# Kernel tuning notes

Measured on AMD Instinct MI355X. Metric: run time of the kernel, lower is better.

The kernel has to match this reference:

```python
import jax, jax.numpy as jnp
import numpy as np

H = 16          # hidden_size
L = 24          # num_layers
LEN_TRAIN = 96
LEN_PRED = 48
B = 256         # leading dim of input (acts as TIME axis for the LSTMs, see notes)


def setup_inputs() -> dict:
    key = jax.random.key(0)
    ks = jax.random.split(key, 16)
    s = 1.0 / np.sqrt(H)  # PyTorch LSTM/Linear init scale
    u = lambda k, shp: jax.random.uniform(k, shp, jnp.float32, -s, s)
    return {
        "x": jax.random.normal(ks[0], (B, 1, LEN_TRAIN), jnp.float32),
        # lstm1: layer0 input_size=1, layers 1..23 input_size=2H
        "W_ih0_1": u(ks[1], (2, 4 * H, 1)),
        "W_ih_1": u(ks[2], (L - 1, 2, 4 * H, 2 * H)),
        "W_hh_1": u(ks[3], (L, 2, 4 * H, H)),
        "b_ih_1": u(ks[4], (L, 2, 4 * H)),
        "b_hh_1": u(ks[5], (L, 2, 4 * H)),
        # lstm2: all layers input_size=2H
        "W_ih_2": u(ks[6], (L, 2, 4 * H, 2 * H)),
        "W_hh_2": u(ks[7], (L, 2, 4 * H, H)),
        "b_ih_2": u(ks[8], (L, 2, 4 * H)),
        "b_hh_2": u(ks[9], (L, 2, 4 * H)),
        "fc1_w": u(ks[10], (1000, 2 * LEN_PRED * H)),
        "fc1_b": u(ks[11], (1000,)),
        "fc2_w": u(ks[12], (LEN_PRED, 1000)),
        "fc2_b": u(ks[13], (LEN_PRED,)),
    }


def _lstm_dir(x, Wih, Whh, bih, bhh, reverse):
    # x: (T, N, in). Precompute input-gate GEMM over whole sequence.
    xg = jnp.einsum("tni,gi->tng", x, Wih) + bih + bhh  # (T, N, 4H)

    def step(carry, g_in):
        h, c = carry
        g = g_in + h @ Whh.T
        i, f, gg, o = jnp.split(g, 4, axis=-1)  # PyTorch gate order i,f,g,o
        c = jax.nn.sigmoid(f) * c + jax.nn.sigmoid(i) * jnp.tanh(gg)
        h = jax.nn.sigmoid(o) * jnp.tanh(c)
        return (h, c), h

    N = x.shape[1]
    init = (jnp.zeros((N, H), x.dtype), jnp.zeros((N, H), x.dtype))
    _, hs = jax.lax.scan(step, init, xg, reverse=reverse)
    return hs  # (T, N, H), in original time order


def _bilstm_stack(x, Wih_per_layer, Whh, bih, bhh):
    for l in range(Whh.shape[0]):
        Wih = Wih_per_layer[l]
        fwd = _lstm_dir(x, Wih[0], Whh[l, 0], bih[l, 0], bhh[l, 0], False)
        bwd = _lstm_dir(x, Wih[1], Whh[l, 1], bih[l, 1], bhh[l, 1], True)
        x = jnp.concatenate([fwd, bwd], axis=-1)  # (T, N, 2H)
    return x


def reference(x, W_ih0_1, W_ih_1, W_hh_1, b_ih_1, b_hh_1,
              W_ih_2, W_hh_2, b_ih_2, b_hh_2,
              fc1_w, fc1_b, fc2_w, fc2_b):
    xp = jnp.transpose(x, (0, 2, 1))  # (B, 96, 1); dim0 is the LSTM time axis (batch_first=False quirk)
    wih1 = [W_ih0_1] + [W_ih_1[i] for i in range(L - 1)]
    h = _bilstm_stack(xp, wih1, W_hh_1, b_ih_1, b_hh_1)      # (B, 96, 2H)
    x1 = h[:, -LEN_PRED:, :]                                  # (B, 48, 2H)
    wih2 = [W_ih_2[i] for i in range(L)]
    h2 = _bilstm_stack(x1, wih2, W_hh_2, b_ih_2, b_hh_2)      # (B, 48, 2H)
    z = h2 + x1
    flat = z.reshape(z.shape[0], -1)                          # (B, 1536)
    y = jax.nn.relu(flat @ fc1_w.T + fc1_b) @ fc2_w.T + fc2_b # (B, 48)
    return jnp.transpose(y.reshape(y.shape[0], LEN_PRED, 1), (0, 2, 1))  # (B, 1, 48)
```

## Files before the change

### kernel.cpp

```cpp
#include <hip/hip_runtime.h>


template <int SEL>
__device__ __forceinline__ float quad_bcast(float v) {
  return __int_as_float(__builtin_amdgcn_update_dpp(
      0, __float_as_int(v), SEL * 0x55, 0xF, 0xF, true));
}

template <int IN_SZ, int N>
__global__ __launch_bounds__(256) void lstm_layer(
    const float* __restrict__ xin, float* __restrict__ xout,
    const float* __restrict__ Wih, const float* __restrict__ Whh,
    const float* __restrict__ bih, const float* __restrict__ bhh,
    int t_stride, int n_off) {
  __shared__ float xg[256 * 64];

  const int tid = threadIdx.x;
  const int lane = tid & 63;
  const int w = tid >> 6;
  const int d = blockIdx.x / N;
  const int n = blockIdx.x % N;

  {
    const int r = lane;
    const float bias = bih[d * 64 + r] + bhh[d * 64 + r];
    if constexpr (IN_SZ == 1) {
      const float xv =
          xin[(size_t)(w * 64 + lane) * t_stride + (n + n_off)];
      const float wih0 = Wih[d * 64 + r];
      const int xvb = __float_as_int(xv);
      for (int ti = 0; ti < 64; ++ti) {
        const float xs = __int_as_float(__builtin_amdgcn_readlane(xvb, ti));
        xg[(w * 64 + ti) * 64 + r] = fmaf(wih0, xs, bias);
      }
    } else {
      const int r8 = lane >> 3;
      const int c = lane & 7;
      const float* gbase = xin + (size_t)(n + n_off) * 32 + c * 4;
      float4 v[8];
#pragma unroll
      for (int i = 0; i < 8; ++i) {
        const int t = w * 64 + i * 8 + r8;
        v[i] = *reinterpret_cast<const float4*>(gbase + (size_t)t * t_stride);
      }
#pragma unroll
      for (int i = 0; i < 8; ++i) {
        const int t = w * 64 + i * 8 + r8;
        *reinterpret_cast<float4*>(&xg[t * 64 + 32 + c * 4]) = v[i];
      }
      float wih[32];
      const float4* wp =
          reinterpret_cast<const float4*>(Wih + (size_t)(d * 64 + r) * 32);
#pragma unroll
      for (int q = 0; q < 8; ++q) {
        const float4 t4 = wp[q];
        wih[4 * q + 0] = t4.x;
        wih[4 * q + 1] = t4.y;
        wih[4 * q + 2] = t4.z;
        wih[4 * q + 3] = t4.w;
      }
      for (int ti = 0; ti < 64; ++ti) {
        const int t = w * 64 + ti;
        const float4* xr = reinterpret_cast<const float4*>(&xg[t * 64 + 32]);
        float a0 = bias, a1 = 0.f, a2 = 0.f, a3 = 0.f;
#pragma unroll
        for (int q = 0; q < 8; ++q) {
          const float4 xv = xr[q];
          a0 = fmaf(wih[4 * q + 0], xv.x, a0);
          a1 = fmaf(wih[4 * q + 1], xv.y, a1);
          a2 = fmaf(wih[4 * q + 2], xv.z, a2);
          a3 = fmaf(wih[4 * q + 3], xv.w, a3);
        }
        xg[t * 64 + r] = (a0 + a1) + (a2 + a3);
      }
    }
  }
  __syncthreads();

  if (w == 0) {
    const int j = lane >> 2;
    const int g = lane & 3;
    const int r = g * 16 + j;

    float whh[16];
#pragma unroll
    for (int k = 0; k < 16; ++k) whh[k] = Whh[(d * 64 + r) * 16 + k];

    const float s_ = (g == 2) ? 2.885390082f : -1.442695041f;
    const float m_ = (g == 2) ? -2.0f : 1.0f;
    const float b_ = (g == 2) ? 1.0f : 0.0f;

    float hs[16];
#pragma unroll
    for (int k = 0; k < 16; ++k) hs[k] = 0.f;
    float c = 0.f;

    const int dt = d ? -1 : 1;
    int t = d ? 255 : 0;
    float cur0 = xg[t * 64 + r];
    float cur1 = xg[(t + dt) * 64 + r];

#define LSTM_STEP(CUR, TT)                                              \
  {                                                                     \
    float a0 = (CUR), a1 = 0.f, a2 = 0.f, a3 = 0.f;                     \
    _Pragma("unroll") for (int k = 0; k < 16; k += 4) {                 \
      a0 = fmaf(whh[k + 0], hs[k + 0], a0);                             \
      a1 = fmaf(whh[k + 1], hs[k + 1], a1);                             \
      a2 = fmaf(whh[k + 2], hs[k + 2], a2);                             \
      a3 = fmaf(whh[k + 3], hs[k + 3], a3);                             \
    }                                                                   \
    const float gv = (a0 + a1) + (a2 + a3);                             \
    const float e = __builtin_amdgcn_exp2f(s_ * gv);                    \
    const float v = fmaf(m_, __builtin_amdgcn_rcpf(1.0f + e), b_);      \
    const float si = quad_bcast<0>(v);                                  \
    const float sf = quad_bcast<1>(v);                                  \
    const float tg = quad_bcast<2>(v);                                  \
    const float so = quad_bcast<3>(v);                                  \
    c = fmaf(sf, c, si * tg);                                           \
    const float e2 = __builtin_amdgcn_exp2f(2.885390082f * c);          \
    const float th = fmaf(-2.0f, __builtin_amdgcn_rcpf(1.0f + e2), 1.0f); \
    const float h = so * th;                                            \
    xg[(TT)*64 + lane] = h;    \
    const int hb = __float_as_int(h);                                   \
    _Pragma("unroll") for (int k = 0; k < 16; ++k) hs[k] =              \
        __int_as_float(__builtin_amdgcn_readlane(hb, 4 * k));           \
  }

    for (int tt = 0; tt < 256; tt += 2) {
      const float nx0 = xg[((t + 2 * dt) & 255) * 64 + r];
      LSTM_STEP(cur0, t)
      const float nx1 = xg[((t + 3 * dt) & 255) * 64 + r];
      LSTM_STEP(cur1, t + dt)
      cur0 = nx0;
      cur1 = nx1;
      t += 2 * dt;
    }
#undef LSTM_STEP
  }
  __syncthreads();

  {
    const int q4 = tid & 3;
    const int tb = tid >> 2;
#pragma unroll
    for (int p = 0; p < 4; ++p) {
      const int t = p * 64 + tb;
      float4 v;
      v.x = xg[t * 64 + 16 * q4 + 0];
      v.y = xg[t * 64 + 16 * q4 + 4];
      v.z = xg[t * 64 + 16 * q4 + 8];
      v.w = xg[t * 64 + 16 * q4 + 12];
      *reinterpret_cast<float4*>(xout + ((size_t)t * N + n) * 32 + d * 16 +
                                 q4 * 4) = v;
    }
  }
}

__global__ __launch_bounds__(256) void fc1_kernel(
    const float* __restrict__ h2,
    const float* __restrict__ x1b,
    const float* __restrict__ w1, const float* __restrict__ b1,
    float* __restrict__ y1) {
  __shared__ float Zs[16][68];
  __shared__ float Ws[16][68];
  const int tid = threadIdx.x;
  const int m0 = blockIdx.x * 64;
  const int b0 = blockIdx.y * 64;
  const int rr = tid >> 2;
  const int c4 = (tid & 3) * 4;
  const int tx = tid & 15, ty = tid >> 4;

  float acc[4][4];
#pragma unroll
  for (int i = 0; i < 4; ++i)
#pragma unroll
    for (int jj = 0; jj < 4; ++jj) acc[i][jj] = 0.f;

  const bool wvalid = (m0 + rr) < 1000;
  const float* zr = h2 + (size_t)(b0 + rr) * 1536 + c4;
  const float* zr2 = x1b + (size_t)(b0 + rr) * 3072 + 1536 + c4;
  const float* wr = w1 + (size_t)(m0 + rr) * 1536 + c4;

  float4 za = *reinterpret_cast<const float4*>(zr);
  float4 zb = *reinterpret_cast<const float4*>(zr2);
  float4 wv = wvalid ? *reinterpret_cast<const float4*>(wr)
                     : make_float4(0.f, 0.f, 0.f, 0.f);

  for (int k0 = 0; k0 < 1536; k0 += 16) {
    Zs[c4 + 0][rr] = za.x + zb.x;
    Zs[c4 + 1][rr] = za.y + zb.y;
    Zs[c4 + 2][rr] = za.z + zb.z;
    Zs[c4 + 3][rr] = za.w + zb.w;
    Ws[c4 + 0][rr] = wv.x;
    Ws[c4 + 1][rr] = wv.y;
    Ws[c4 + 2][rr] = wv.z;
    Ws[c4 + 3][rr] = wv.w;
    if (k0 + 16 < 1536) {
      za = *reinterpret_cast<const float4*>(zr + k0 + 16);
      zb = *reinterpret_cast<const float4*>(zr2 + k0 + 16);
      if (wvalid) wv = *reinterpret_cast<const float4*>(wr + k0 + 16);
    }
    __syncthreads();
#pragma unroll
    for (int kk = 0; kk < 16; ++kk) {
      const float4 av = *reinterpret_cast<const float4*>(&Zs[kk][ty * 4]);
      const float4 bv = *reinterpret_cast<const float4*>(&Ws[kk][tx * 4]);
      const float a_[4] = {av.x, av.y, av.z, av.w};
      const float b_[4] = {bv.x, bv.y, bv.z, bv.w};
#pragma unroll
      for (int i = 0; i < 4; ++i)
#pragma unroll
        for (int jj = 0; jj < 4; ++jj)
          acc[i][jj] = fmaf(a_[i], b_[jj], acc[i][jj]);
    }
    __syncthreads();
  }
#pragma unroll
  for (int i = 0; i < 4; ++i) {
    const int b = b0 + ty * 4 + i;
#pragma unroll
    for (int jj = 0; jj < 4; ++jj) {
      const int m = m0 + tx * 4 + jj;
      if (m < 1000) {
        float vo = acc[i][jj] + b1[m];
        y1[(size_t)b * 1000 + m] = vo > 0.f ? vo : 0.f;
      }
    }
  }
}

__global__ __launch_bounds__(64) void fc2_kernel(
    const float* __restrict__ y1, const float* __restrict__ w2,
    const float* __restrict__ b2, float* __restrict__ out) {
  __shared__ float ys[1000];
  const int b = blockIdx.x;
  for (int k = threadIdx.x; k < 1000; k += 64) ys[k] = y1[(size_t)b * 1000 + k];
  __syncthreads();
  const int p = threadIdx.x;
  if (p < 48) {
    float a0 = b2[p], a1 = 0.f, a2 = 0.f, a3 = 0.f;
    const float* wr = w2 + (size_t)p * 1000;
    for (int k = 0; k < 1000; k += 4) {
      const float4 wv = *reinterpret_cast<const float4*>(wr + k);
      a0 = fmaf(ys[k + 0], wv.x, a0);
      a1 = fmaf(ys[k + 1], wv.y, a1);
      a2 = fmaf(ys[k + 2], wv.z, a2);
      a3 = fmaf(ys[k + 3], wv.w, a3);
    }
    out[(size_t)b * 48 + p] = (a0 + a1) + (a2 + a3);
  }
}

extern "C" void kernel_launch(void* const* d_in, const int* in_sizes, int n_in,
                              void* d_out, int out_size, void* d_ws,
                              size_t ws_size, hipStream_t stream) {
  const float* x = (const float*)d_in[0];
  const float* W_ih0_1 = (const float*)d_in[1];
  const float* W_ih_1 = (const float*)d_in[2];
  const float* W_hh_1 = (const float*)d_in[3];
  const float* b_ih_1 = (const float*)d_in[4];
  const float* b_hh_1 = (const float*)d_in[5];
  const float* W_ih_2 = (const float*)d_in[6];
  const float* W_hh_2 = (const float*)d_in[7];
  const float* b_ih_2 = (const float*)d_in[8];
  const float* b_hh_2 = (const float*)d_in[9];
  const float* fc1_w = (const float*)d_in[10];
  const float* fc1_b = (const float*)d_in[11];
  const float* fc2_w = (const float*)d_in[12];
  const float* fc2_b = (const float*)d_in[13];

  float* ws = (float*)d_ws;
  float* buf0 = ws;
  float* buf1 = ws + 786432;
  float* y1 = ws + 2 * 786432;
  float* q0 = buf0;
  float* q1 = buf0 + 393216;

  lstm_layer<1, 96><<<192, 256, 0, stream>>>(x, buf0, W_ih0_1, W_hh_1, b_ih_1,
                                             b_hh_1, 96, 0);
  for (int l = 1; l < 24; ++l) {
    const float* in = (l & 1) ? buf0 : buf1;
    float* outb = (l & 1) ? buf1 : buf0;
    lstm_layer<32, 96><<<192, 256, 0, stream>>>(
        in, outb, W_ih_1 + (size_t)(l - 1) * 4096, W_hh_1 + (size_t)l * 2048,
        b_ih_1 + l * 128, b_hh_1 + l * 128, 3072, 0);
  }
  lstm_layer<32, 48><<<96, 256, 0, stream>>>(buf1, q0, W_ih_2, W_hh_2, b_ih_2,
                                             b_hh_2, 3072, 48);
  for (int l = 1; l < 24; ++l) {
    const float* in = (l & 1) ? q0 : q1;
    float* outb = (l & 1) ? q1 : q0;
    lstm_layer<32, 48><<<96, 256, 0, stream>>>(
        in, outb, W_ih_2 + (size_t)l * 4096, W_hh_2 + (size_t)l * 2048,
        b_ih_2 + l * 128, b_hh_2 + l * 128, 1536, 0);
  }
  fc1_kernel<<<dim3(16, 4), 256, 0, stream>>>(q1, buf1, fc1_w, fc1_b, y1);
  fc2_kernel<<<256, 64, 0, stream>>>(y1, fc2_w, fc2_b, (float*)d_out);
}
```

Before: 2.238 ms.

## Fuse all LSTM layers into one persistent kernel and compute only needed columns

Replaces 48 per-layer LSTM launches with a single kernel where each block handles one of the 48 columns actually consumed downstream, running both directions and all layers with activations kept in LDS. Input-gate projections for the next layer are computed in-block from LDS instead of reloading from global memory. This removes launch overhead, global round trips, and the unused half of the first stack's columns, at the cost of only 48 blocks of parallelism.

Measured after the change: 3.063 ms. 1.37x slower.

```diff
diff --git a/kernel.cpp b/kernel.cpp
--- a/kernel.cpp
+++ b/kernel.cpp
@@ -7,158 +7,204 @@
       0, __float_as_int(v), SEL * 0x55, 0xF, 0xF, true));
 }
 
-template <int IN_SZ, int N>
-__global__ __launch_bounds__(256) void lstm_layer(
-    const float* __restrict__ xin, float* __restrict__ xout,
-    const float* __restrict__ Wih, const float* __restrict__ Whh,
-    const float* __restrict__ bih, const float* __restrict__ bhh,
-    int t_stride, int n_off) {
-  __shared__ float xg[256 * 64];
+__global__ __launch_bounds__(512) void lstm_fused(
+    const float* __restrict__ x, const float* __restrict__ W_ih0_1,
+    const float* __restrict__ W_ih_1, const float* __restrict__ W_hh_1,
+    const float* __restrict__ b_ih_1, const float* __restrict__ b_hh_1,
+    const float* __restrict__ W_ih_2, const float* __restrict__ W_hh_2,
+    const float* __restrict__ b_ih_2, const float* __restrict__ b_hh_2,
+    float* __restrict__ x1out, float* __restrict__ h2out) {
+  __shared__ float xgF[256 * 64];
+  __shared__ float xgB[256 * 64];
 
   const int tid = threadIdx.x;
   const int lane = tid & 63;
   const int w = tid >> 6;
-  const int d = blockIdx.x / N;
-  const int n = blockIdx.x % N;
+  const int np = blockIdx.x;
+  const int nglob = 48 + np;
 
   {
+    const int d = w >> 2;
+    const int wv = w & 3;
+    float* xg = d ? xgB : xgF;
     const int r = lane;
-    const float bias = bih[d * 64 + r] + bhh[d * 64 + r];
-    if constexpr (IN_SZ == 1) {
-      const float xv =
-          xin[(size_t)(w * 64 + lane) * t_stride + (n + n_off)];
-      const float wih0 = Wih[d * 64 + r];
-      const int xvb = __float_as_int(xv);
-      for (int ti = 0; ti < 64; ++ti) {
-        const float xs = __int_as_float(__builtin_amdgcn_readlane(xvb, ti));
-        xg[(w * 64 + ti) * 64 + r] = fmaf(wih0, xs, bias);
-      }
-    } else {
-      const int r8 = lane >> 3;
-      const int c = lane & 7;
-      const float* gbase = xin + (size_t)(n + n_off) * 32 + c * 4;
-      float4 v[8];
-#pragma unroll
-      for (int i = 0; i < 8; ++i) {
-        const int t = w * 64 + i * 8 + r8;
-        v[i] = *reinterpret_cast<const float4*>(gbase + (size_t)t * t_stride);
-      }
-#pragma unroll
-      for (int i = 0; i < 8; ++i) {
-        const int t = w * 64 + i * 8 + r8;
-        *reinterpret_cast<float4*>(&xg[t * 64 + 32 + c * 4]) = v[i];
-      }
-      float wih[32];
-      const float4* wp =
-          reinterpret_cast<const float4*>(Wih + (size_t)(d * 64 + r) * 32);
-#pragma unroll
-      for (int q = 0; q < 8; ++q) {
-        const float4 t4 = wp[q];
-        wih[4 * q + 0] = t4.x;
-        wih[4 * q + 1] = t4.y;
-        wih[4 * q + 2] = t4.z;
-        wih[4 * q + 3] = t4.w;
-      }
-      for (int ti = 0; ti < 64; ++ti) {
-        const int t = w * 64 + ti;
-        const float4* xr = reinterpret_cast<const float4*>(&xg[t * 64 + 32]);
-        float a0 = bias, a1 = 0.f, a2 = 0.f, a3 = 0.f;
+    const float bias = b_ih_1[d * 64 + r] + b_hh_1[d * 64 + r];
+    const float wih0 = W_ih0_1[d * 64 + r];
+    const int xvb =
+        __float_as_int(x[(size_t)(wv * 64 + lane) * 96 + nglob]);
+    for (int ti = 0; ti < 64; ++ti) {
+      const float xs = __int_as_float(__builtin_amdgcn_readlane(xvb, ti));
+      xg[(wv * 64 + ti) * 64 + r] = fmaf(wih0, xs, bias);
+    }
+  }
+  __syncthreads();
+
+  for (int L = 0; L < 48; ++L) {
+    if ((w & 3) == 0) {
+      const int d = w >> 2;
+      float* xg = d ? xgB : xgF;
+      const int j = lane >> 2;
+      const int g = lane & 3;
+      const int r = g * 16 + j;
+
+      const float* WhhP =
+          ((L < 24) ? (W_hh_1 + (size_t)L * 2048)
+                    : (W_hh_2 + (size_t)(L - 24) * 2048)) +
+          (size_t)d * 1024 + (size_t)r * 16;
+      float whh[16];
+#pragma unroll
+      for (int k = 0; k < 16; ++k) whh[k] = WhhP[k];
+
+      const float s_ = (g == 2) ? 2.885390082f : -1.442695041f;
+      const float m_ = (g == 2) ? -2.0f : 1.0f;
+      const float b_ = (g == 2) ? 1.0f : 0.0f;
+
+      float hs[16];
+#pragma unroll
+      for (int k = 0; k < 16; ++k) hs[k] = 0.f;
+      float c = 0.f;
+
+      const int dt = d ? -1 : 1;
+      int t = d ? 255 : 0;
+      float cur0 = xg[t * 64 + r];
+      float cur1 = xg[(t + dt) * 64 + r];
+
+#define LSTM_STEP(CUR, TT)                                                \
+  {                                                                       \
+    float a0 = (CUR), a1 = 0.f, a2 = 0.f, a3 = 0.f;                       \
+    _Pragma("unroll") for (int k = 0; k < 16; k += 4) {                   \
+      a0 = fmaf(whh[k + 0], hs[k + 0], a0);                               \
+      a1 = fmaf(whh[k + 1], hs[k + 1], a1);                               \
+      a2 = fmaf(whh[k + 2], hs[k + 2], a2);                               \
+      a3 = fmaf(whh[k + 3], hs[k + 3], a3);                               \
+    }                                                                     \
+    const float gv = (a0 + a1) + (a2 + a3);                               \
+    const float e = __builtin_amdgcn_exp2f(s_ * gv);                      \
+    const float v = fmaf(m_, __builtin_amdgcn_rcpf(1.0f + e), b_);        \
+    const float si = quad_bcast<0>(v);                                    \
+    const float sf = quad_bcast<1>(v);                                    \
+    const float tg = quad_bcast<2>(v);                                    \
+    const float so = quad_bcast<3>(v);                                    \
+    c = fmaf(sf, c, si * tg);                                             \
+    const float e2 = __builtin_amdgcn_exp2f(2.885390082f * c);            \
+    const float th = fmaf(-2.0f, __builtin_amdgcn_rcpf(1.0f + e2), 1.0f); \
+    const float h = so * th;                                              \
+    xg[(TT)*64 + r] = h;  \
+    const int hb = __float_as_int(h);                                     \
+    _Pragma("unroll") for (int k = 0; k < 16; ++k) hs[k] =                \
+        __int_as_float(__builtin_amdgcn_readlane(hb, 4 * k));             \
+  }
+
+      for (int tt = 0; tt < 256; tt += 2) {
+        const float nx0 = xg[((t + 2 * dt) & 255) * 64 + r];
+        LSTM_STEP(cur0, t)
+        const float nx1 = xg[((t + 3 * dt) & 255) * 64 + r];
+        LSTM_STEP(cur1, t + dt)
+        cur0 = nx0;
+        cur1 = nx1;
+        t += 2 * dt;
+      }
+#undef LSTM_STEP
+    }
+    __syncthreads();
+
+    if (L == 23 || L == 47) {
+      float* dst = (L == 23) ? x1out : h2out;
+#pragma unroll
+      for (int p = 0; p < 4; ++p) {
+        const int gi = p * 512 + tid;
+        const int t = gi >> 3;
+        const int cc = gi & 7;
+        const float* src = (cc < 4) ? &xgF[t * 64 + cc * 4]
+                                    : &xgB[t * 64 + (cc - 4) * 4];
+        const float4 v = *reinterpret_cast<const float4*>(src);
+        *reinterpret_cast<float4*>(dst + ((size_t)t * 48 + np) * 32 +
+                                   cc * 4) = v;
+      }
+      if (L == 47) break;
+      __syncthreads();
+    }
+
+    {
+      const int M = L + 1;
+      const float* WihP;
+      const float* bihP;
+      const float* bhhP;
+      if (M < 24) {
+        WihP = W_ih_1 + (size_t)(M - 1) * 4096;
+        bihP = b_ih_1 + (size_t)M * 128;
+        bhhP = b_hh_1 + (size_t)M * 128;
+      } else {
+        WihP = W_ih_2 + (size_t)(M - 24) * 4096;
+        bihP = b_ih_2 + (size_t)(M - 24) * 128;
+        bhhP = b_hh_2 + (size_t)(M - 24) * 128;
+      }
+      const int r = lane;
+      const float biasF = bihP[r] + bhhP[r];
+      const float biasB = bihP[64 + r] + bhhP[64 + r];
+
+      float wf[32], wb[32];
+      {
+        const float4* pf =
+            reinterpret_cast<const float4*>(WihP + (size_t)r * 32);
+        const float4* pb =
+            reinterpret_cast<const float4*>(WihP + 2048 + (size_t)r * 32);
 #pragma unroll
         for (int q = 0; q < 8; ++q) {
-          const float4 xv = xr[q];
-          a0 = fmaf(wih[4 * q + 0], xv.x, a0);
-          a1 = fmaf(wih[4 * q + 1], xv.y, a1);
-          a2 = fmaf(wih[4 * q + 2], xv.z, a2);
-          a3 = fmaf(wih[4 * q + 3], xv.w, a3);
+          const float4 a = pf[q];
+          wf[4 * q + 0] = a.x;
+          wf[4 * q + 1] = a.y;
+          wf[4 * q + 2] = a.z;
+          wf[4 * q + 3] = a.w;
+          const float4 b = pb[q];
+          wb[4 * q + 0] = b.x;
+          wb[4 * q + 1] = b.y;
+          wb[4 * q + 2] = b.z;
+          wb[4 * q + 3] = b.w;
         }
-        xg[t * 64 + r] = (a0 + a1) + (a2 + a3);
-      }
-    }
-  }
-  __syncthreads();
-
-  if (w == 0) {
-    const int j = lane >> 2;
-    const int g = lane & 3;
-    const int r = g * 16 + j;
-
-    float whh[16];
-#pragma unroll
-    for (int k = 0; k < 16; ++k) whh[k] = Whh[(d * 64 + r) * 16 + k];
-
-    const float s_ = (g == 2) ? 2.885390082f : -1.442695041f;
-    const float m_ = (g == 2) ? -2.0f : 1.0f;
-    const float b_ = (g == 2) ? 1.0f : 0.0f;
-
-    float hs[16];
-#pragma unroll
-    for (int k = 0; k < 16; ++k) hs[k] = 0.f;
-    float c = 0.f;
-
-    const int dt = d ? -1 : 1;
-    int t = d ? 255 : 0;
-    float cur0 = xg[t * 64 + r];
-    float cur1 = xg[(t + dt) * 64 + r];
-
-#define LSTM_STEP(CUR, TT)                                              \
-  {                                                                     \
-    float a0 = (CUR), a1 = 0.f, a2 = 0.f, a3 = 0.f;                     \
-    _Pragma("unroll") for (int k = 0; k < 16; k += 4) {                 \
-      a0 = fmaf(whh[k + 0], hs[k + 0], a0);                             \
-      a1 = fmaf(whh[k + 1], hs[k + 1], a1);                             \
-      a2 = fmaf(whh[k + 2], hs[k + 2], a2);                             \
-      a3 = fmaf(whh[k + 3], hs[k + 3], a3);                             \
-    }                                                                   \
-    const float gv = (a0 + a1) + (a2 + a3);                             \
-    const float e = __builtin_amdgcn_exp2f(s_ * gv);                    \
-    const float v = fmaf(m_, __builtin_amdgcn_rcpf(1.0f + e), b_);      \
-    const float si = quad_bcast<0>(v);                                  \
-    const float sf = quad_bcast<1>(v);                                  \
-    const float tg = quad_bcast<2>(v);                                  \
-    const float so = quad_bcast<3>(v);                                  \
-    c = fmaf(sf, c, si * tg);                                           \
-    const float e2 = __builtin_amdgcn_exp2f(2.885390082f * c);          \
-    const float th = fmaf(-2.0f, __builtin_amdgcn_rcpf(1.0f + e2), 1.0f); \
-    const float h = so * th;                                            \
-    xg[(TT)*64 + lane] = h;    \
-    const int hb = __float_as_int(h);                                   \
-    _Pragma("unroll") for (int k = 0; k < 16; ++k) hs[k] =              \
-        __int_as_float(__builtin_amdgcn_readlane(hb, 4 * k));           \
-  }
-
-    for (int tt = 0; tt < 256; tt += 2) {
-      const float nx0 = xg[((t + 2 * dt) & 255) * 64 + r];
-      LSTM_STEP(cur0, t)
-      const float nx1 = xg[((t + 3 * dt) & 255) * 64 + r];
-      LSTM_STEP(cur1, t + dt)
-      cur0 = nx0;
-      cur1 = nx1;
-      t += 2 * dt;
-    }
-#undef LSTM_STEP
-  }
-  __syncthreads();
-
-  {
-    const int q4 = tid & 3;
-    const int tb = tid >> 2;
-#pragma unroll
-    for (int p = 0; p < 4; ++p) {
-      const int t = p * 64 + tb;
-      float4 v;
-      v.x = xg[t * 64 + 16 * q4 + 0];
-      v.y = xg[t * 64 + 16 * q4 + 4];
-      v.z = xg[t * 64 + 16 * q4 + 8];
-      v.w = xg[t * 64 + 16 * q4 + 12];
-      *reinterpret_cast<float4*>(xout + ((size_t)t * N + n) * 32 + d * 16 +
-                                 q4 * 4) = v;
-    }
+      }
+
+      for (int ti = 0; ti < 32; ++ti) {
+        const int t = w * 32 + ti;
+        const float4* qf = reinterpret_cast<const float4*>(&xgF[t * 64]);
+        const float4* qb = reinterpret_cast<const float4*>(&xgB[t * 64]);
+        float xv[32];
+#pragma unroll
+        for (int q = 0; q < 4; ++q) {
+          const float4 a = qf[q];
+          xv[4 * q + 0] = a.x;
+          xv[4 * q + 1] = a.y;
+          xv[4 * q + 2] = a.z;
+          xv[4 * q + 3] = a.w;
+          const float4 b = qb[q];
+          xv[16 + 4 * q + 0] = b.x;
+          xv[16 + 4 * q + 1] = b.y;
+          xv[16 + 4 * q + 2] = b.z;
+          xv[16 + 4 * q + 3] = b.w;
+        }
+        float f0 = biasF, f1 = 0.f, f2 = 0.f, f3 = 0.f;
+        float g0 = biasB, g1 = 0.f, g2 = 0.f, g3 = 0.f;
+#pragma unroll
+        for (int k = 0; k < 32; k += 4) {
+          f0 = fmaf(wf[k + 0], xv[k + 0], f0);
+          f1 = fmaf(wf[k + 1], xv[k + 1], f1);
+          f2 = fmaf(wf[k + 2], xv[k + 2], f2);
+          f3 = fmaf(wf[k + 3], xv[k + 3], f3);
+          g0 = fmaf(wb[k + 0], xv[k + 0], g0);
+          g1 = fmaf(wb[k + 1], xv[k + 1], g1);
+          g2 = fmaf(wb[k + 2], xv[k + 2], g2);
+          g3 = fmaf(wb[k + 3], xv[k + 3], g3);
+        }
+        xgF[t * 64 + lane] = (f0 + f1) + (f2 + f3);
+        xgB[t * 64 + lane] = (g0 + g1) + (g2 + g3);
+      }
+    }
+    __syncthreads();
   }
 }
 
 __global__ __launch_bounds__(256) void fc1_kernel(
-    const float* __restrict__ h2,
-    const float* __restrict__ x1b,
+    const float* __restrict__ h2, const float* __restrict__ x1b,
     const float* __restrict__ w1, const float* __restrict__ b1,
     float* __restrict__ y1) {
   __shared__ float Zs[16][68];
@@ -178,7 +224,7 @@
 
   const bool wvalid = (m0 + rr) < 1000;
   const float* zr = h2 + (size_t)(b0 + rr) * 1536 + c4;
-  const float* zr2 = x1b + (size_t)(b0 + rr) * 3072 + 1536 + c4;
+  const float* zr2 = x1b + (size_t)(b0 + rr) * 1536 + c4;
   const float* wr = w1 + (size_t)(m0 + rr) * 1536 + c4;
 
   float4 za = *reinterpret_cast<const float4*>(zr);
@@ -270,30 +316,13 @@
   const float* fc2_b = (const float*)d_in[13];
 
   float* ws = (float*)d_ws;
-  float* buf0 = ws;
-  float* buf1 = ws + 786432;
-  float* y1 = ws + 2 * 786432;
-  float* q0 = buf0;
-  float* q1 = buf0 + 393216;
-
-  lstm_layer<1, 96><<<192, 256, 0, stream>>>(x, buf0, W_ih0_1, W_hh_1, b_ih_1,
-                                             b_hh_1, 96, 0);
-  for (int l = 1; l < 24; ++l) {
-    const float* in = (l & 1) ? buf0 : buf1;
-    float* outb = (l & 1) ? buf1 : buf0;
-    lstm_layer<32, 96><<<192, 256, 0, stream>>>(
-        in, outb, W_ih_1 + (size_t)(l - 1) * 4096, W_hh_1 + (size_t)l * 2048,
-        b_ih_1 + l * 128, b_hh_1 + l * 128, 3072, 0);
-  }
-  lstm_layer<32, 48><<<96, 256, 0, stream>>>(buf1, q0, W_ih_2, W_hh_2, b_ih_2,
-                                             b_hh_2, 3072, 48);
-  for (int l = 1; l < 24; ++l) {
-    const float* in = (l & 1) ? q0 : q1;
-    float* outb = (l & 1) ? q1 : q0;
-    lstm_layer<32, 48><<<96, 256, 0, stream>>>(
-        in, outb, W_ih_2 + (size_t)l * 4096, W_hh_2 + (size_t)l * 2048,
-        b_ih_2 + l * 128, b_hh_2 + l * 128, 1536, 0);
-  }
-  fc1_kernel<<<dim3(16, 4), 256, 0, stream>>>(q1, buf1, fc1_w, fc1_b, y1);
+  float* x1b = ws;
+  float* h2b = ws + 393216;
+  float* y1 = ws + 786432;
+
+  lstm_fused<<<48, 512, 0, stream>>>(x, W_ih0_1, W_ih_1, W_hh_1, b_ih_1,
+                                     b_hh_1, W_ih_2, W_hh_2, b_ih_2, b_hh_2,
+                                     x1b, h2b);
+  fc1_kernel<<<dim3(16, 4), 256, 0, stream>>>(h2b, x1b, fc1_w, fc1_b, y1);
   fc2_kernel<<<256, 64, 0, stream>>>(y1, fc2_w, fc2_b, (float*)d_out);
 }
```
